# Performance work log

Hardware: AMD Instinct MI355X
Metric: run time of the kernel (lower is better)

The kernel has to match this reference:

```python
import jax, jax.numpy as jnp
import numpy as np

B, S, D, H = 4, 2048, 512, 8
DH = D // H  # depth per head = 64


def setup_inputs() -> dict:
    key = jax.random.key(0)
    ks = jax.random.split(key, 8)
    scale = 1.0 / np.sqrt(D)
    return {
        "query": jax.random.normal(ks[0], (B, S, D), jnp.float32),
        "key": jax.random.normal(ks[1], (B, S, D), jnp.float32),
        "value": jax.random.normal(ks[2], (B, S, D), jnp.float32),
        "mask": jax.random.randint(ks[3], (B, S), 0, 2, jnp.int32),
        "wq_w": jax.random.normal(ks[4], (D, D), jnp.float32) * scale,
        "wq_b": jnp.zeros((D,), jnp.float32),
        "wk_w": jax.random.normal(ks[5], (D, D), jnp.float32) * scale,
        "wk_b": jnp.zeros((D,), jnp.float32),
        "wv_w": jax.random.normal(ks[6], (D, D), jnp.float32) * scale,
        "wv_b": jnp.zeros((D,), jnp.float32),
        "wo_w": jax.random.normal(ks[7], (D, D), jnp.float32) * scale,
        "wo_b": jnp.zeros((D,), jnp.float32),
    }


def _split_heads(x):
    # [B, S, D] -> [B, H, S, DH]
    b, s, _ = x.shape
    return x.reshape(b, s, H, DH).transpose(0, 2, 1, 3)


def reference(query, key, value, mask, wq_w, wq_b, wk_w, wk_b, wv_w, wv_b, wo_w, wo_b):
    q = _split_heads(query @ wq_w + wq_b)   # [B,H,S,DH]
    k = _split_heads(key @ wk_w + wk_b)
    v = _split_heads(value @ wv_w + wv_b)

    scale = 1.0 / jnp.sqrt(jnp.asarray(DH, jnp.float32))
    logits = jnp.einsum('bhqd,bhkd->bhqk', q, k) * scale  # [B,H,S,S]
    # additive key-padding mask: 1 -> masked (adds -1e9)
    m = mask.astype(logits.dtype)[:, None, None, :]  # [B,1,1,S]
    logits = logits + m * -1e9
    weights = jax.nn.softmax(logits, axis=-1)
    attn = jnp.einsum('bhqk,bhkd->bhqd', weights, v)  # [B,H,S,DH]
    attn = attn.transpose(0, 2, 1, 3).reshape(query.shape[0], -1, D)  # [B,S,D]
    return attn @ wo_w + wo_b
```

## Files before the change

kernel.cpp:

```cpp
#include <hip/hip_runtime.h>
#include <stdint.h>

#define QSCALE (0.125f * 1.44269504088896340736f)
#define MASKNEG (-1.442695e9f)

typedef unsigned short u16;
typedef unsigned int u32;
typedef __bf16 bf16x8 __attribute__((ext_vector_type(8)));
typedef __bf16 bf16x4 __attribute__((ext_vector_type(4)));
typedef float f32x4 __attribute__((ext_vector_type(4)));
typedef u16 u16x8 __attribute__((ext_vector_type(8)));

__device__ __forceinline__ u16 f2bf(float f) {
  u32 u = __float_as_uint(f);
  u += 0x7fffu + ((u >> 16) & 1u);
  return (u16)(u >> 16);
}

__device__ __forceinline__ void gload16(const void* src, void* ldsbase) {
  __builtin_amdgcn_global_load_lds(
      (const __attribute__((address_space(1))) u32*)src,
      (__attribute__((address_space(3))) u32*)ldsbase, 16, 0, 0);
}

__global__ __launch_bounds__(256) void conv_in(const float* __restrict__ q,
                                               const float* __restrict__ k,
                                               const float* __restrict__ v,
                                               u16* __restrict__ dst) {
  const float* src = (blockIdx.z == 0) ? q : (blockIdx.z == 1) ? k : v;
  u16* d = dst + (size_t)blockIdx.z * 4194304;
  size_t i = ((size_t)blockIdx.x * 256 + threadIdx.x) * 8;
  float4 a = *(const float4*)(src + i);
  float4 b = *(const float4*)(src + i + 4);
  u16x8 ov;
  ov[0] = f2bf(a.x); ov[1] = f2bf(a.y); ov[2] = f2bf(a.z); ov[3] = f2bf(a.w);
  ov[4] = f2bf(b.x); ov[5] = f2bf(b.y); ov[6] = f2bf(b.z); ov[7] = f2bf(b.w);
  *(u16x8*)(d + i) = ov;
}

__global__ __launch_bounds__(256) void conv_w(const float* __restrict__ wq,
                                              const float* __restrict__ wk,
                                              const float* __restrict__ wv,
                                              const float* __restrict__ wo,
                                              u16* __restrict__ wT) {
  const float* src = (blockIdx.z == 0) ? wq : (blockIdx.z == 1) ? wk
                    : (blockIdx.z == 2) ? wv : wo;
  u16* dst = wT + (size_t)blockIdx.z * 262144;
  __shared__ float t[64][65];
  const int n0 = blockIdx.x * 64, k0 = blockIdx.y * 64;
  const int lr = threadIdx.x >> 6, lc = threadIdx.x & 63;
#pragma unroll
  for (int it = 0; it < 16; ++it) {
    const int row = it * 4 + lr;
    t[row][lc] = src[(size_t)(k0 + row) * 512 + n0 + lc];
  }
  __syncthreads();
#pragma unroll
  for (int it = 0; it < 16; ++it) {
    const int row = it * 4 + lr;
    dst[(size_t)(n0 + row) * 512 + k0 + lc] = f2bf(t[lc][row]);
  }
}

__device__ __forceinline__ void gemm_core(const u16* __restrict__ A,
                                          const u16* __restrict__ Bt,
                                          int m0, int n0, char* lds,
                                          f32x4 acc[4][4]) {
  const int tid = threadIdx.x;
  const int lane = tid & 63;
  const int wave = tid >> 6;
  const int wm = wave >> 1, wn = wave & 1;
  const int srow = tid >> 3;
  const int sc16 = tid & 7;

  auto stage = [&](int buf, int kt) {
    const int k0 = kt * 64;
    char* base = lds + buf * 32768;
#pragma unroll
    for (int c = 0; c < 4; ++c) {
      const int row = c * 32 + srow;
      const int xc = (sc16 ^ (row & 7)) << 3;
      gload16(A + (size_t)(m0 + row) * 512 + k0 + xc,
              base + c * 4096 + (wave << 10));
      gload16(Bt + (size_t)(n0 + row) * 512 + k0 + xc,
              base + 16384 + c * 4096 + (wave << 10));
    }
  };

  auto compute = [&](int buf) {
    const char* bA = lds + buf * 32768;
    const char* bB = bA + 16384;
#pragma unroll
    for (int kk = 0; kk < 2; ++kk) {
      const int c16 = kk * 4 + (lane >> 4);
      bf16x8 av[4], bv[4];
#pragma unroll
      for (int i = 0; i < 4; ++i) {
        const int row = wm * 64 + i * 16 + (lane & 15);
        av[i] = *(const bf16x8*)(bA + row * 128 + ((c16 ^ (row & 7)) << 4));
      }
#pragma unroll
      for (int j = 0; j < 4; ++j) {
        const int row = wn * 64 + j * 16 + (lane & 15);
        bv[j] = *(const bf16x8*)(bB + row * 128 + ((c16 ^ (row & 7)) << 4));
      }
#pragma unroll
      for (int i = 0; i < 4; ++i)
#pragma unroll
        for (int j = 0; j < 4; ++j)
          acc[i][j] = __builtin_amdgcn_mfma_f32_16x16x32_bf16(av[i], bv[j],
                                                              acc[i][j], 0, 0, 0);
    }
  };

  stage(0, 0);
  __syncthreads();
#pragma unroll
  for (int kt = 0; kt < 8; ++kt) {
    const int cur = kt & 1;
    if (kt < 7) stage(cur ^ 1, kt + 1);
    compute(cur);
    __syncthreads();
  }
}

__global__ __launch_bounds__(256) void gemm_qkv(
    const u16* __restrict__ xq, const u16* __restrict__ xk,
    const u16* __restrict__ xv, const u16* __restrict__ wT,
    const float* __restrict__ bq, const float* __restrict__ bk,
    const float* __restrict__ bv, u16* __restrict__ qws, u16* __restrict__ kws,
    u16* __restrict__ vTw) {
  __shared__ __align__(16) char lds[65536];
  const int z = blockIdx.z;
  const u16* A = (z == 0) ? xq : (z == 1) ? xk : xv;
  const u16* Bt = wT + (size_t)z * 262144;
  const float* bias = (z == 0) ? bq : (z == 1) ? bk : bv;
  const int m0 = blockIdx.y * 128, n0 = blockIdx.x * 128;
  f32x4 acc[4][4] = {};
  gemm_core(A, Bt, m0, n0, lds, acc);
  const int lane = threadIdx.x & 63, wave = threadIdx.x >> 6;
  const int wm = wave >> 1, wn = wave & 1;
#pragma unroll
  for (int j = 0; j < 4; ++j) {
    const int n = n0 + wn * 64 + j * 16 + (lane & 15);
    const float bn = bias[n];
    const int h = n >> 6, dh = n & 63;
#pragma unroll
    for (int i = 0; i < 4; ++i) {
#pragma unroll
      for (int r = 0; r < 4; ++r) {
        const int rg = m0 + wm * 64 + i * 16 + ((lane >> 4) << 2) + r;
        const int b = rg >> 11, s = rg & 2047;
        const int bh = b * 8 + h;
        const float val = acc[i][j][r] + bn;
        if (z == 0) {
          qws[((size_t)bh * 2048 + s) * 64 + dh] = f2bf(val * QSCALE);
        } else if (z == 1) {
          kws[((size_t)bh * 2048 + s) * 64 + dh] = f2bf(val);
        } else {
          vTw[((size_t)bh * 64 + dh) * 2048 + s] = f2bf(val);
        }
      }
    }
  }
}

__global__ __launch_bounds__(512, 4) void attn_fwd(
    const u16* __restrict__ qws, const u16* __restrict__ kws,
    const u16* __restrict__ vTw, const int* __restrict__ mask,
    u16* __restrict__ attn) {
  __shared__ __align__(16) char ldsK[32768];
  __shared__ __align__(16) char ldsV[32768];
  __shared__ __align__(16) char plds[16384];
  const int qt = blockIdx.x;
  const int bh = blockIdx.y;
  const int b = bh >> 3;
  const int tid = threadIdx.x;
  const int lane = tid & 63, wave = tid >> 6;
  const int half = wave >> 2, wl = wave & 3;
  const int hi = lane >> 4;
  const int q15 = lane & 15;

  const int rb = q15 * 128;
  const int xorb = (lane & 7) << 4;
  const int kx0 = ((hi) ^ (lane & 7)) << 4;
  const int kx1 = ((4 + hi) ^ (lane & 7)) << 4;
  const int px0 = (hi * 16) ^ xorb;
  const int px1 = (64 + hi * 16) ^ xorb;

  const u16* qbase = qws + ((size_t)bh * 2048 + qt * 64 + wl * 16) * 64;
  bf16x8 qa[2];
#pragma unroll
  for (int kk = 0; kk < 2; ++kk)
    qa[kk] = *(const bf16x8*)(qbase + q15 * 64 + kk * 32 + hi * 8);

  char* myK = ldsK + half * 16384;
  char* myV = ldsV + half * 16384;
  const int srow = wl * 8 + (lane >> 3);
  const int sc16 = lane & 7;

  auto stage = [&](int buf, int ktg) {
#pragma unroll
    for (int c = 0; c < 2; ++c) {
      const int row = c * 32 + srow;
      const int xc = (sc16 ^ (row & 7)) << 3;
      gload16(kws + ((size_t)bh * 2048 + ktg * 64 + row) * 64 + xc,
              myK + buf * 8192 + c * 4096 + (wl << 10));
      gload16(vTw + ((size_t)bh * 64 + row) * 2048 + ktg * 64 + xc,
              myV + buf * 8192 + c * 4096 + (wl << 10));
    }
  };

  float rs = 0.f;
  f32x4 o[4] = {};
  char* pw = plds + wave * 2048;

  stage(0, half * 16);
  __syncthreads();

  for (int kt = 0; kt < 16; ++kt) {
    const int cur = kt & 1;
    const int ktg = half * 16 + kt;

    int4 mm[4];
#pragma unroll
    for (int t = 0; t < 4; ++t)
      mm[t] = *(const int4*)(mask + b * 2048 + ktg * 64 + t * 16 + hi * 4);

    if (kt < 15) stage(cur ^ 1, ktg + 1);

    const char* kb = myK + cur * 8192;
    f32x4 sv[4] = {};
    __builtin_amdgcn_s_setprio(1);
#pragma unroll
    for (int t = 0; t < 4; ++t) {
      const bf16x8 kf0 = *(const bf16x8*)(kb + t * 2048 + rb + kx0);
      const bf16x8 kf1 = *(const bf16x8*)(kb + t * 2048 + rb + kx1);
      sv[t] = __builtin_amdgcn_mfma_f32_16x16x32_bf16(kf0, qa[0], sv[t], 0, 0, 0);
      sv[t] = __builtin_amdgcn_mfma_f32_16x16x32_bf16(kf1, qa[1], sv[t], 0, 0, 0);
    }
    __builtin_amdgcn_s_setprio(0);

#pragma unroll
    for (int t = 0; t < 4; ++t) {
      const int mmv[4] = {mm[t].x, mm[t].y, mm[t].z, mm[t].w};
      bf16x4 pk;
#pragma unroll
      for (int r = 0; r < 4; ++r) {
        const float p =
            __builtin_amdgcn_exp2f(sv[t][r] + (mmv[r] ? MASKNEG : 0.0f));
        rs += p;
        pk[r] = (__bf16)p;
      }
      *(bf16x4*)(pw + rb + ((t * 32 + hi * 8) ^ xorb)) = pk;
    }

    const char* vb = myV + cur * 8192;
    __builtin_amdgcn_s_setprio(1);
#pragma unroll
    for (int kk = 0; kk < 2; ++kk) {
      const bf16x8 pa = *(const bf16x8*)(pw + rb + (kk ? px1 : px0));
#pragma unroll
      for (int dt = 0; dt < 4; ++dt) {
        const bf16x8 vf =
            *(const bf16x8*)(vb + dt * 2048 + rb + (kk ? kx1 : kx0));
        o[dt] = __builtin_amdgcn_mfma_f32_16x16x32_bf16(pa, vf, o[dt], 0, 0, 0);
      }
    }
    __builtin_amdgcn_s_setprio(0);
    __syncthreads();
  }

  float lred = rs;
  lred += __shfl_xor(lred, 16);
  lred += __shfl_xor(lred, 32);
  float lq[4];
#pragma unroll
  for (int r = 0; r < 4; ++r) lq[r] = __shfl(lred, hi * 4 + r);

  float* oSh = (float*)ldsK;
  float* lSh = (float*)ldsV;
  if (half == 1) {
#pragma unroll
    for (int dt = 0; dt < 4; ++dt)
#pragma unroll
      for (int r = 0; r < 4; ++r)
        oSh[wl * 1024 + (hi * 4 + r) * 64 + dt * 16 + q15] = o[dt][r];
    if (hi == 0) lSh[wl * 16 + q15] = lred;
  }
  __syncthreads();
  if (half == 0) {
    const int h = bh & 7;
    float invl[4];
#pragma unroll
    for (int r = 0; r < 4; ++r)
      invl[r] = 1.0f / (lq[r] + lSh[wl * 16 + hi * 4 + r]);
    const int sq0 = qt * 64 + wl * 16 + hi * 4;
#pragma unroll
    for (int dt = 0; dt < 4; ++dt) {
      const int dcol = h * 64 + dt * 16 + q15;
#pragma unroll
      for (int r = 0; r < 4; ++r) {
        const float val =
            (o[dt][r] + oSh[wl * 1024 + (hi * 4 + r) * 64 + dt * 16 + q15]) *
            invl[r];
        attn[(size_t)(b * 2048 + sq0 + r) * 512 + dcol] = f2bf(val);
      }
    }
  }
}

__global__ __launch_bounds__(256) void gemm_out(const u16* __restrict__ attn,
                                                const u16* __restrict__ woT,
                                                const float* __restrict__ bo,
                                                float* __restrict__ out) {
  __shared__ __align__(16) char lds[65536];
  const int m0 = blockIdx.y * 128, n0 = blockIdx.x * 128;
  f32x4 acc[4][4] = {};
  gemm_core(attn, woT, m0, n0, lds, acc);
  const int lane = threadIdx.x & 63, wave = threadIdx.x >> 6;
  const int wm = wave >> 1, wn = wave & 1;
#pragma unroll
  for (int j = 0; j < 4; ++j) {
    const int n = n0 + wn * 64 + j * 16 + (lane & 15);
    const float bn = bo[n];
#pragma unroll
    for (int i = 0; i < 4; ++i) {
      const int rbase = m0 + wm * 64 + i * 16 + ((lane >> 4) << 2);
#pragma unroll
      for (int r = 0; r < 4; ++r)
        out[(size_t)(rbase + r) * 512 + n] = acc[i][j][r] + bn;
    }
  }
}

extern "C" void kernel_launch(void* const* d_in, const int* in_sizes, int n_in,
                              void* d_out, int out_size, void* d_ws,
                              size_t ws_size, hipStream_t stream) {
  (void)in_sizes; (void)n_in; (void)out_size; (void)ws_size;
  const float* q = (const float*)d_in[0];
  const float* k = (const float*)d_in[1];
  const float* v = (const float*)d_in[2];
  const int* mask = (const int*)d_in[3];
  const float* wq = (const float*)d_in[4];
  const float* bq = (const float*)d_in[5];
  const float* wk = (const float*)d_in[6];
  const float* bk = (const float*)d_in[7];
  const float* wv = (const float*)d_in[8];
  const float* bv = (const float*)d_in[9];
  const float* wo = (const float*)d_in[10];
  const float* bo = (const float*)d_in[11];

  u16* xq = (u16*)d_ws;
  u16* xk = xq + 4194304;
  u16* xv = xk + 4194304;
  u16* wT = xv + 4194304;
  u16* qws = wT + 1048576;
  u16* kws = qws + 4194304;
  u16* vTw = kws + 4194304;
  u16* attn = xq;
  float* out = (float*)d_out;

  conv_in<<<dim3(2048, 1, 3), 256, 0, stream>>>(q, k, v, xq);
  conv_w<<<dim3(8, 8, 4), 256, 0, stream>>>(wq, wk, wv, wo, wT);
  gemm_qkv<<<dim3(4, 64, 3), 256, 0, stream>>>(xq, xk, xv, wT, bq, bk, bv, qws,
                                               kws, vTw);
  attn_fwd<<<dim3(32, 32), 512, 0, stream>>>(qws, kws, vTw, mask, attn);
  gemm_out<<<dim3(4, 64), 256, 0, stream>>>(attn, wT + 786432, bo, out);
}
```

Before: 123.2 us.

## Rework attention kernel with 32x32 MFMA, register-resident P and LDS mask bias

Moves the attention inner loop from 16x16x32 to 32x32x16 bf16 MFMA, so each block now handles 128 query rows instead of 64 and the grid is halved and reordered. The probabilities are packed in registers with v_cvt_pk_bf16_f32 and v_permlane32_swap instead of round-tripping through LDS. The mask is preloaded once as an additive bias in LDS and used as the MFMA accumulator init. Synchronisation now uses explicit vmcnt waits and raw barriers, and the epilogue stores vectorised bf16 rows. This should cut LDS traffic and instruction count, at the cost of more registers and therefore possibly lower occupancy.

```diff
diff --git a/kernel.cpp b/kernel.cpp
--- a/kernel.cpp
+++ b/kernel.cpp
@@ -7,14 +7,25 @@
 typedef unsigned short u16;
 typedef unsigned int u32;
 typedef __bf16 bf16x8 __attribute__((ext_vector_type(8)));
-typedef __bf16 bf16x4 __attribute__((ext_vector_type(4)));
 typedef float f32x4 __attribute__((ext_vector_type(4)));
+typedef float f32x16 __attribute__((ext_vector_type(16)));
 typedef u16 u16x8 __attribute__((ext_vector_type(8)));
+typedef u32 u32x4 __attribute__((ext_vector_type(4)));
 
 __device__ __forceinline__ u16 f2bf(float f) {
   u32 u = __float_as_uint(f);
   u += 0x7fffu + ((u >> 16) & 1u);
   return (u16)(u >> 16);
+}
+
+__device__ __forceinline__ u32 cvtpk(float lo, float hi) {
+  u32 d;
+  asm("v_cvt_pk_bf16_f32 %0, %1, %2" : "=v"(d) : "v"(lo), "v"(hi));
+  return d;
+}
+
+__device__ __forceinline__ void plswap(u32& a, u32& b) {
+  asm("v_permlane32_swap_b32 %0, %1" : "+v"(a), "+v"(b));
 }
 
 __device__ __forceinline__ void gload16(const void* src, void* ldsbase) {
@@ -171,28 +182,38 @@
     u16* __restrict__ attn) {
   __shared__ __align__(16) char ldsK[32768];
   __shared__ __align__(16) char ldsV[32768];
-  __shared__ __align__(16) char plds[16384];
-  const int qt = blockIdx.x;
-  const int bh = blockIdx.y;
+  __shared__ __align__(16) float biasLDS[2048];
+  __shared__ float lSh[256];
+
+  const int bh = blockIdx.x;
+  const int qt = blockIdx.y;
   const int b = bh >> 3;
   const int tid = threadIdx.x;
   const int lane = tid & 63, wave = tid >> 6;
   const int half = wave >> 2, wl = wave & 3;
-  const int hi = lane >> 4;
-  const int q15 = lane & 15;
-
-  const int rb = q15 * 128;
-  const int xorb = (lane & 7) << 4;
-  const int kx0 = ((hi) ^ (lane & 7)) << 4;
-  const int kx1 = ((4 + hi) ^ (lane & 7)) << 4;
-  const int px0 = (hi * 16) ^ xorb;
-  const int px1 = (64 + hi * 16) ^ xorb;
-
-  const u16* qbase = qws + ((size_t)bh * 2048 + qt * 64 + wl * 16) * 64;
-  bf16x8 qa[2];
-#pragma unroll
-  for (int kk = 0; kk < 2; ++kk)
-    qa[kk] = *(const bf16x8*)(qbase + q15 * 64 + kk * 32 + hi * 8);
+  const int l31 = lane & 31, h5 = lane >> 5;
+
+  {
+    const int4 m4 = *(const int4*)(mask + b * 2048 + tid * 4);
+    float4 bv;
+    bv.x = m4.x ? MASKNEG : 0.0f;
+    bv.y = m4.y ? MASKNEG : 0.0f;
+    bv.z = m4.z ? MASKNEG : 0.0f;
+    bv.w = m4.w ? MASKNEG : 0.0f;
+    *(float4*)(biasLDS + tid * 4) = bv;
+  }
+  asm volatile("s_waitcnt lgkmcnt(0)" ::: "memory");
+
+  const u16* qrow_p = qws + ((size_t)bh * 2048 + qt * 128 + wl * 32 + l31) * 64;
+  bf16x8 qb[4];
+#pragma unroll
+  for (int c = 0; c < 4; ++c)
+    qb[c] = *(const bf16x8*)(qrow_p + c * 16 + h5 * 8);
+
+  const int rowb = l31 * 128;
+  int kxs[4];
+#pragma unroll
+  for (int c = 0; c < 4; ++c) kxs[c] = ((2 * c + h5) ^ (l31 & 7)) << 4;
 
   char* myK = ldsK + half * 16384;
   char* myV = ldsV + half * 16384;
@@ -211,102 +232,107 @@
     }
   };
 
-  float rs = 0.f;
-  f32x4 o[4] = {};
-  char* pw = plds + wave * 2048;
+  f32x16 o0 = {}, o1 = {};
+  float rsp0 = 0.f, rsp1 = 0.f, rsp2 = 0.f, rsp3 = 0.f;
+
+  auto do_subtile = [&](const char* kb, const char* vb, const float* biasT,
+                        int stByte, int c0) {
+    f32x16 sv;
+#pragma unroll
+    for (int g = 0; g < 4; ++g) {
+      const f32x4 bq4 = *(const f32x4*)(biasT + g * 8 + h5 * 4);
+      sv[g * 4 + 0] = bq4[0];
+      sv[g * 4 + 1] = bq4[1];
+      sv[g * 4 + 2] = bq4[2];
+      sv[g * 4 + 3] = bq4[3];
+    }
+    __builtin_amdgcn_s_setprio(1);
+#pragma unroll
+    for (int c = 0; c < 4; ++c) {
+      const bf16x8 kf = *(const bf16x8*)(kb + stByte + rowb + kxs[c]);
+      sv = __builtin_amdgcn_mfma_f32_32x32x16_bf16(kf, qb[c], sv, 0, 0, 0);
+    }
+    __builtin_amdgcn_s_setprio(0);
+    float p[16];
+#pragma unroll
+    for (int i = 0; i < 16; ++i) p[i] = __builtin_amdgcn_exp2f(sv[i]);
+    rsp0 += p[0] + p[4] + p[8] + p[12];
+    rsp1 += p[1] + p[5] + p[9] + p[13];
+    rsp2 += p[2] + p[6] + p[10] + p[14];
+    rsp3 += p[3] + p[7] + p[11] + p[15];
+    u32 paw[2][4];
+#pragma unroll
+    for (int lc = 0; lc < 2; ++lc) {
+      u32 a1 = cvtpk(p[lc * 8 + 0], p[lc * 8 + 1]);
+      u32 b1 = cvtpk(p[lc * 8 + 4], p[lc * 8 + 5]);
+      u32 a2 = cvtpk(p[lc * 8 + 2], p[lc * 8 + 3]);
+      u32 b2 = cvtpk(p[lc * 8 + 6], p[lc * 8 + 7]);
+      plswap(a1, b1);
+      plswap(a2, b2);
+      paw[lc][0] = a1; paw[lc][1] = a2; paw[lc][2] = b1; paw[lc][3] = b2;
+    }
+    __builtin_amdgcn_s_setprio(1);
+#pragma unroll
+    for (int lc = 0; lc < 2; ++lc) {
+      u32x4 w = {paw[lc][0], paw[lc][1], paw[lc][2], paw[lc][3]};
+      const bf16x8 pa = __builtin_bit_cast(bf16x8, w);
+      const bf16x8 vf0 = *(const bf16x8*)(vb + rowb + kxs[c0 + lc]);
+      o0 = __builtin_amdgcn_mfma_f32_32x32x16_bf16(pa, vf0, o0, 0, 0, 0);
+      const bf16x8 vf1 = *(const bf16x8*)(vb + 4096 + rowb + kxs[c0 + lc]);
+      o1 = __builtin_amdgcn_mfma_f32_32x32x16_bf16(pa, vf1, o1, 0, 0, 0);
+    }
+    __builtin_amdgcn_s_setprio(0);
+  };
 
   stage(0, half * 16);
-  __syncthreads();
 
   for (int kt = 0; kt < 16; ++kt) {
     const int cur = kt & 1;
     const int ktg = half * 16 + kt;
-
-    int4 mm[4];
-#pragma unroll
-    for (int t = 0; t < 4; ++t)
-      mm[t] = *(const int4*)(mask + b * 2048 + ktg * 64 + t * 16 + hi * 4);
-
-    if (kt < 15) stage(cur ^ 1, ktg + 1);
-
+    if (kt < 15) {
+      stage(cur ^ 1, ktg + 1);
+      asm volatile("s_waitcnt vmcnt(4)" ::: "memory");
+    } else {
+      asm volatile("s_waitcnt vmcnt(0)" ::: "memory");
+    }
+    __builtin_amdgcn_sched_barrier(0);
+    __builtin_amdgcn_s_barrier();
     const char* kb = myK + cur * 8192;
-    f32x4 sv[4] = {};
-    __builtin_amdgcn_s_setprio(1);
-#pragma unroll
-    for (int t = 0; t < 4; ++t) {
-      const bf16x8 kf0 = *(const bf16x8*)(kb + t * 2048 + rb + kx0);
-      const bf16x8 kf1 = *(const bf16x8*)(kb + t * 2048 + rb + kx1);
-      sv[t] = __builtin_amdgcn_mfma_f32_16x16x32_bf16(kf0, qa[0], sv[t], 0, 0, 0);
-      sv[t] = __builtin_amdgcn_mfma_f32_16x16x32_bf16(kf1, qa[1], sv[t], 0, 0, 0);
-    }
-    __builtin_amdgcn_s_setprio(0);
-
-#pragma unroll
-    for (int t = 0; t < 4; ++t) {
-      const int mmv[4] = {mm[t].x, mm[t].y, mm[t].z, mm[t].w};
-      bf16x4 pk;
-#pragma unroll
-      for (int r = 0; r < 4; ++r) {
-        const float p =
-            __builtin_amdgcn_exp2f(sv[t][r] + (mmv[r] ? MASKNEG : 0.0f));
-        rs += p;
-        pk[r] = (__bf16)p;
-      }
-      *(bf16x4*)(pw + rb + ((t * 32 + hi * 8) ^ xorb)) = pk;
-    }
-
     const char* vb = myV + cur * 8192;
-    __builtin_amdgcn_s_setprio(1);
-#pragma unroll
-    for (int kk = 0; kk < 2; ++kk) {
-      const bf16x8 pa = *(const bf16x8*)(pw + rb + (kk ? px1 : px0));
-#pragma unroll
-      for (int dt = 0; dt < 4; ++dt) {
-        const bf16x8 vf =
-            *(const bf16x8*)(vb + dt * 2048 + rb + (kk ? kx1 : kx0));
-        o[dt] = __builtin_amdgcn_mfma_f32_16x16x32_bf16(pa, vf, o[dt], 0, 0, 0);
-      }
-    }
-    __builtin_amdgcn_s_setprio(0);
-    __syncthreads();
-  }
-
-  float lred = rs;
-  lred += __shfl_xor(lred, 16);
-  lred += __shfl_xor(lred, 32);
-  float lq[4];
-#pragma unroll
-  for (int r = 0; r < 4; ++r) lq[r] = __shfl(lred, hi * 4 + r);
-
-  float* oSh = (float*)ldsK;
-  float* lSh = (float*)ldsV;
-  if (half == 1) {
-#pragma unroll
-    for (int dt = 0; dt < 4; ++dt)
-#pragma unroll
-      for (int r = 0; r < 4; ++r)
-        oSh[wl * 1024 + (hi * 4 + r) * 64 + dt * 16 + q15] = o[dt][r];
-    if (hi == 0) lSh[wl * 16 + q15] = lred;
-  }
+    const float* biasT = biasLDS + ktg * 64;
+    do_subtile(kb, vb, biasT, 0, 0);
+    do_subtile(kb, vb, biasT + 32, 4096, 2);
+    __builtin_amdgcn_sched_barrier(0);
+    __builtin_amdgcn_s_barrier();
+  }
+
+  float rs = (rsp0 + rsp1) + (rsp2 + rsp3);
+  rs += __shfl_xor(rs, 32);
+
+  float* oSh = (float*)(half ? (void*)ldsV : (void*)ldsK);
+#pragma unroll
+  for (int reg = 0; reg < 16; ++reg) {
+    const int q = (reg & 3) + 8 * (reg >> 2) + 4 * h5;
+    oSh[wl * 2048 + q * 64 + l31] = o0[reg];
+    oSh[wl * 2048 + q * 64 + 32 + l31] = o1[reg];
+  }
+  if (h5 == 0) lSh[half * 128 + wl * 32 + l31] = rs;
   __syncthreads();
-  if (half == 0) {
-    const int h = bh & 7;
-    float invl[4];
-#pragma unroll
-    for (int r = 0; r < 4; ++r)
-      invl[r] = 1.0f / (lq[r] + lSh[wl * 16 + hi * 4 + r]);
-    const int sq0 = qt * 64 + wl * 16 + hi * 4;
-#pragma unroll
-    for (int dt = 0; dt < 4; ++dt) {
-      const int dcol = h * 64 + dt * 16 + q15;
-#pragma unroll
-      for (int r = 0; r < 4; ++r) {
-        const float val =
-            (o[dt][r] + oSh[wl * 1024 + (hi * 4 + r) * 64 + dt * 16 + q15]) *
-            invl[r];
-        attn[(size_t)(b * 2048 + sq0 + r) * 512 + dcol] = f2bf(val);
-      }
-    }
+
+  const int h = bh & 7;
+#pragma unroll
+  for (int i = 0; i < 2; ++i) {
+    const int idx = tid + i * 512;
+    const int row = idx >> 3;
+    const int c8 = (idx & 7) * 8;
+    const float inv = 1.0f / (lSh[row] + lSh[128 + row]);
+    const float* A = (const float*)ldsK + row * 64 + c8;
+    const float* Bp = (const float*)ldsV + row * 64 + c8;
+    u16x8 ovv;
+#pragma unroll
+    for (int j = 0; j < 8; ++j) ovv[j] = f2bf((A[j] + Bp[j]) * inv);
+    const int grow = b * 2048 + qt * 128 + row;
+    *(u16x8*)(attn + (size_t)grow * 512 + h * 64 + c8) = ovv;
   }
 }
 
@@ -365,6 +391,6 @@
   conv_w<<<dim3(8, 8, 4), 256, 0, stream>>>(wq, wk, wv, wo, wT);
   gemm_qkv<<<dim3(4, 64, 3), 256, 0, stream>>>(xq, xk, xv, wT, bq, bk, bv, qws,
                                                kws, vTw);
-  attn_fwd<<<dim3(32, 32), 512, 0, stream>>>(qws, kws, vTw, mask, attn);
+  attn_fwd<<<dim3(32, 16), 512, 0, stream>>>(qws, kws, vTw, mask, attn);
   gemm_out<<<dim3(4, 64), 256, 0, stream>>>(attn, wT + 786432, bo, out);
 }
```

Result: faster. 104.4 us (-15.3%).
